# Kernel tuning notes

Hardware: AMD Instinct MI355X
Metric: run time of the kernel (lower is better)

## Reference

```python
import jax, jax.numpy as jnp
import numpy as np

N_NODES = 50000
N_EDGES = 800000
N_FEAT = 128
NHID = 64
B = 512          # num graphs
K = 30           # sort-pool k
N_CLASSES = 10


def _sage(x, src, dst, Wl, bl, Wr, n):
    # PyG SAGEConv: out = lin_l(mean_{j in N(i)} x_j) + lin_r(x_i)
    deg = jax.ops.segment_sum(jnp.ones(src.shape[0], x.dtype), dst, num_segments=n)
    agg = jax.ops.segment_sum(x[src], dst, num_segments=n)
    agg = agg / jnp.maximum(deg, 1.0)[:, None]
    return agg @ Wl + bl + x @ Wr


def _sort_pool(x, batch, num_graphs, k):
    # sort nodes within each graph descending by last feature channel, keep top-k (zero pad)
    n, f = x.shape
    order = jnp.lexsort((-x[:, -1], batch))  # primary: batch asc, secondary: last-feat desc
    xs = x[order]
    bs = batch[order]
    counts = jax.ops.segment_sum(jnp.ones(n, jnp.int32), batch, num_segments=num_graphs)
    starts = jnp.concatenate([jnp.zeros(1, jnp.int32), jnp.cumsum(counts)[:-1]])
    rank = jnp.arange(n, dtype=jnp.int32) - starts[bs]
    valid = rank < k
    gidx = jnp.where(valid, bs, num_graphs)  # out-of-bounds -> dropped by scatter
    ridx = jnp.where(valid, rank, 0)
    out = jnp.zeros((num_graphs, k, f), x.dtype).at[gidx, ridx].set(xs)
    return out  # [B, k, f]


def setup_inputs() -> dict:
    key = jax.random.key(0)
    ks = jax.random.split(key, 16)
    d = {}
    d["x"] = jax.random.normal(ks[0], (N_NODES, N_FEAT), dtype=jnp.float32)
    d["edge_index"] = jax.random.randint(ks[1], (2, N_EDGES), 0, N_NODES, dtype=jnp.int64)
    d["batch"] = jnp.sort(jax.random.randint(ks[2], (N_NODES,), 0, B, dtype=jnp.int64))

    def lin(k, fan_in, shape):
        s = 1.0 / np.sqrt(fan_in)
        return jax.random.uniform(k, shape, jnp.float32, -s, s)

    d["W1l"] = lin(ks[3], N_FEAT, (N_FEAT, NHID)); d["b1"] = lin(ks[4], N_FEAT, (NHID,))
    d["W1r"] = lin(ks[5], N_FEAT, (N_FEAT, NHID))
    d["W2l"] = lin(ks[6], NHID, (NHID, NHID)); d["b2"] = lin(ks[7], NHID, (NHID,))
    d["W2r"] = lin(ks[8], NHID, (NHID, NHID))
    d["W3l"] = lin(ks[9], NHID, (NHID, NHID)); d["b3"] = lin(ks[10], NHID, (NHID,))
    d["W3r"] = lin(ks[11], NHID, (NHID, NHID))
    d["convw"] = lin(ks[12], NHID * 5, (32, NHID, 5))  # OIH
    d["convb"] = lin(ks[13], NHID * 5, (32,))
    d["lin1w"] = lin(ks[14], 32 * 26, (32 * 26, NHID)); d["lin1b"] = lin(ks[14], 32 * 26, (NHID,))
    d["lin2w"] = lin(ks[15], NHID, (NHID, N_CLASSES)); d["lin2b"] = lin(ks[15], NHID, (N_CLASSES,))
    return d


def reference(x, edge_index, batch, W1l, b1, W1r, W2l, b2, W2r, W3l, b3, W3r,
              convw, convb, lin1w, lin1b, lin2w, lin2b):
    src, dst = edge_index[0], edge_index[1]
    h = jax.nn.relu(_sage(x, src, dst, W1l, b1, W1r, N_NODES))
    h = jax.nn.relu(_sage(h, src, dst, W2l, b2, W2r, N_NODES))
    h = jax.nn.relu(_sage(h, src, dst, W3l, b3, W3r, N_NODES))
    p = _sort_pool(h, batch, B, K)            # [B, K, NHID]
    p = jnp.transpose(p, (0, 2, 1))           # [B, NHID, K]
    c = jax.lax.conv_general_dilated(p, convw, (1,), 'VALID',
                                     dimension_numbers=('NCH', 'OIH', 'NCH'))
    c = jax.nn.relu(c + convb[None, :, None])  # [B, 32, 26]
    f = c.reshape(B, -1)
    f = jax.nn.relu(f @ lin1w + lin1b)
    logits = f @ lin2w + lin2b
    return jax.nn.log_softmax(logits, axis=-1)
```

## Files before the change

### kernel.cpp

```cpp
#include <hip/hip_runtime.h>
#include <hip/hip_bf16.h>
#include <math.h>

#define NND 50000
#define NE 800000
#define NF 128
#define NH 64
#define NB 512
#define KP 30
#define NCLS 10
#define NBKT 49
#define NTILE 196
#define NG1 782
#define NSET 208

typedef __hip_bfloat16 bf16;
typedef unsigned long long u64;
typedef unsigned short ushort_t;
typedef __attribute__((ext_vector_type(8))) short bf16x8;
typedef __attribute__((ext_vector_type(4))) float f32x4;

__device__ __forceinline__ float ldF(const void* p, size_t i, int isbf){
    return isbf ? __bfloat162float(((const bf16*)p)[i]) : ((const float*)p)[i];
}

__device__ __forceinline__ ushort_t f2bf(float v){
    unsigned u = __float_as_uint(v);
    unsigned r = u + 0x7FFFu + ((u >> 16) & 1u);
    return (ushort_t)(r >> 16);
}

__device__ __forceinline__ int floatsAreBf16(const unsigned* __restrict__ xw, int tid){
    unsigned w = xw[tid & 63];
    int ex = (int)((w >> 7) & 0xFF);
    u64 m = __ballot(ex >= 100 && ex <= 140);
    return __popcll(m) >= 32;
}
__device__ __forceinline__ int intsAreI64(const int* __restrict__ ew, int tid){
    u64 m = __ballot(ew[2*(tid & 63) + 1] == 0);
    return __popcll(m) >= 48;
}

__device__ __forceinline__ int edgeSrc(const int* ei, int e, int i64){
    return i64 ? ei[2*e] : ei[e];
}
__device__ __forceinline__ int edgeDst(const int* ei, int e, int i64){
    return i64 ? ei[2*NE + 2*e] : ei[NE + e];
}

__global__ __launch_bounds__(256) void k1_kernel(
    const unsigned* __restrict__ xw, const int* __restrict__ ei,
    const int* __restrict__ batch, int* __restrict__ starts,
    const void* W1l, const void* W1r, const void* b1,
    const void* W2l, const void* W2r, const void* b2,
    const void* W3l, const void* W3r, const void* b3,
    const void* convw, const void* convb,
    const void* l1w, const void* l1b, const void* l2w, const void* l2b,
    ushort_t* __restrict__ wB1, ushort_t* __restrict__ wB2, ushort_t* __restrict__ wB3,
    float* __restrict__ b1f, float* __restrict__ b2f, float* __restrict__ b3f,
    float* __restrict__ wT, float* __restrict__ cbf,
    float* __restrict__ l1wf, float* __restrict__ l1bf,
    float* __restrict__ l2wf, float* __restrict__ l2bf,
    int* __restrict__ bcnt, int* __restrict__ dctr,
    int* __restrict__ bbase, int* __restrict__ bcur, int* __restrict__ offs)
{
    int tid = threadIdx.x;
    if (blockIdx.x < NTILE){
        __shared__ int lh[NBKT];
        __shared__ int sc[NBKT];
        __shared__ int lastFlag;
        int i64 = intsAreI64(ei, tid);
        if (tid < NBKT) lh[tid] = 0;
        __syncthreads();
        int t0 = blockIdx.x*4096;
        #pragma unroll 4
        for (int k = 0; k < 16; ++k){
            int e = t0 + k*256 + tid;
            if (e < NE) atomicAdd(&lh[edgeDst(ei,e,i64) >> 10], 1);
        }
        __syncthreads();
        if (tid < NBKT && lh[tid]) atomicAdd(&bcnt[tid], lh[tid]);
        __syncthreads();
        if (tid == 0){
            __threadfence();
            int old = atomicAdd(dctr, 1);
            lastFlag = (old == NTILE-1) ? 1 : 0;
        }
        __syncthreads();
        if (lastFlag){
            if (tid < NBKT) sc[tid] = atomicAdd(&bcnt[tid], 0);
            __syncthreads();
            if (tid == 0){
                int acc = 0;
                for (int b = 0; b < NBKT; ++b){
                    bbase[b] = acc; bcur[b] = acc; acc += sc[b];
                }
                bbase[NBKT] = acc;
                offs[NND] = NE;
            }
        }
    } else {
        int wbf = floatsAreBf16(xw, tid);
        int i64 = intsAreI64(ei, tid);
        int i = (blockIdx.x - NTILE)*256 + tid;
        if (i < NND){
            int b  = i64 ? batch[2*i] : batch[i];
            int pb = (i == 0) ? -1 : (i64 ? batch[2*(i-1)] : batch[i-1]);
            for (int g = pb+1; g <= b; ++g) starts[g] = i;
            if (i == NND-1) for (int g = b+1; g <= NB; ++g) starts[g] = NND;
        }
        {
            int j = i & 7, lane = (i >> 3) & 63, t = (i >> 9) & 7, c = i >> 12;
            int k = c*32 + (lane >> 4)*8 + j;
            int n = t*16 + (lane & 15);
            if (i < 16384){
                float v = (n < 64) ? ldF(W1l, (size_t)k*NH + n, wbf)
                                   : ldF(W1r, (size_t)k*NH + (n-64), wbf);
                wB1[i] = f2bf(v);
            }
            if (i < 8192){
                float v2 = (n < 64) ? ldF(W2l, (size_t)k*NH + n, wbf)
                                    : ldF(W2r, (size_t)k*NH + (n-64), wbf);
                float v3 = (n < 64) ? ldF(W3l, (size_t)k*NH + n, wbf)
                                    : ldF(W3r, (size_t)k*NH + (n-64), wbf);
                wB2[i] = f2bf(v2);
                wB3[i] = f2bf(v3);
            }
        }
        if (i < 64){
            b1f[i] = ldF(b1, i, wbf);
            b2f[i] = ldF(b2, i, wbf);
            b3f[i] = ldF(b3, i, wbf);
            l1bf[i] = ldF(l1b, i, wbf);
        }
        if (i < 10240){
            int o = i / 320, rem = i - o*320, ch = rem/5, h = rem - ch*5;
            wT[ch*160 + h*32 + o] = ldF(convw, i, wbf);
        }
        if (i < 53248) l1wf[i] = ldF(l1w, i, wbf);
        if (i < 640)   l2wf[i] = ldF(l2w, i, wbf);
        if (i < 32)    cbf[i]  = ldF(convb, i, wbf);
        if (i < 10)    l2bf[i] = ldF(l2b, i, wbf);
    }
}

__global__ __launch_bounds__(256) void k2_kernel(
    const void* __restrict__ x, const int* __restrict__ ei,
    const ushort_t* __restrict__ wB1, const float* __restrict__ b1f,
    ushort_t* __restrict__ ybf, float* __restrict__ z,
    int* __restrict__ bcur, int2* __restrict__ bedges)
{
    int tid = threadIdx.x;
    if (blockIdx.x < NG1){
        constexpr int K = NF, KC = K/32, RS = K + 8;
        __shared__ ushort_t hA[64*RS];
        int isbf = floatsAreBf16((const unsigned*)x, tid);
        int base = blockIdx.x * 64;
        for (int i = tid; i < 64*K; i += 256){
            int r = i / K, c = i - r*K;
            int node = base + r;
            float v = (node < NND) ? ldF(x, (size_t)node*K + c, isbf) : 0.f;
            hA[r*RS + c] = f2bf(v);
        }
        __syncthreads();
        int lane = tid & 63, w = tid >> 6;
        int n16 = lane & 15, quad = lane >> 4;
        f32x4 acc[8];
        #pragma unroll
        for (int t = 0; t < 8; ++t) acc[t] = (f32x4){0.f,0.f,0.f,0.f};
        const bf16x8* bp = (const bf16x8*)wB1;
        #pragma unroll
        for (int c = 0; c < KC; ++c){
            bf16x8 a = *(const bf16x8*)&hA[(w*16 + n16)*RS + c*32 + quad*8];
            #pragma unroll
            for (int t = 0; t < 8; ++t){
                bf16x8 b = bp[(c*8 + t)*64 + lane];
                acc[t] = __builtin_amdgcn_mfma_f32_16x16x32_bf16(a, b, acc[t], 0, 0, 0);
            }
        }
        #pragma unroll
        for (int t = 0; t < 8; ++t){
            int f = (t & 3)*16 + n16;
            float bv = (t >= 4) ? b1f[f] : 0.f;
            #pragma unroll
            for (int r = 0; r < 4; ++r){
                int node = base + w*16 + quad*4 + r;
                if (node < NND){
                    if (t < 4) ybf[(size_t)node*NH + f] = f2bf(acc[t][r]);
                    else       z[(size_t)node*NH + f] = acc[t][r] + bv;
                }
            }
        }
    } else {
        __shared__ int lh[NBKT];
        __shared__ int lcur[NBKT];
        int i64 = intsAreI64(ei, tid);
        if (tid < NBKT) lh[tid] = 0;
        __syncthreads();
        int t0 = (blockIdx.x - NG1)*4096;
        int myd[16], mys[16];
        int cnt = 0;
        #pragma unroll 4
        for (int k = 0; k < 16; ++k){
            int e = t0 + k*256 + tid;
            if (e < NE){
                int d = edgeDst(ei,e,i64), s_ = edgeSrc(ei,e,i64);
                myd[cnt] = d; mys[cnt] = s_; ++cnt;
                atomicAdd(&lh[d >> 10], 1);
            }
        }
        __syncthreads();
        if (tid < NBKT) lcur[tid] = lh[tid] ? atomicAdd(&bcur[tid], lh[tid]) : 0;
        __syncthreads();
        for (int k = 0; k < cnt; ++k){
            int b = myd[k] >> 10;
            int p = atomicAdd(&lcur[b], 1);
            bedges[p] = make_int2(mys[k], myd[k]);
        }
    }
}

__global__ __launch_bounds__(1024) void csr_finalize(const int2* __restrict__ bedges,
                                                     const int* __restrict__ bbase,
                                                     int* __restrict__ offs,
                                                     int* __restrict__ csr){
    __shared__ int hist[1024];
    int b = blockIdx.x;
    int tid = threadIdx.x;
    int dst0 = b << 10;
    int nd = NND - dst0; if (nd > 1024) nd = 1024;
    int e0 = bbase[b], e1 = bbase[b+1];
    hist[tid] = 0;
    __syncthreads();
    for (int e = e0 + tid; e < e1; e += 1024)
        atomicAdd(&hist[bedges[e].y - dst0], 1);
    __syncthreads();
    int own = hist[tid];
    for (int st = 1; st < 1024; st <<= 1){
        int v = (tid >= st) ? hist[tid-st] : 0;
        __syncthreads();
        hist[tid] += v;
        __syncthreads();
    }
    int excl = hist[tid] - own;
    if (tid < nd) offs[dst0 + tid] = e0 + excl;
    __syncthreads();
    hist[tid] = excl;
    __syncthreads();
    for (int e = e0 + tid; e < e1; e += 1024){
        int2 ed = bedges[e];
        int p = atomicAdd(&hist[ed.y - dst0], 1);
        csr[e0 + p] = ed.x;
    }
}

__device__ __forceinline__ void addbf8(uint4 u, float* a){
    a[0] += __uint_as_float(u.x << 16);
    a[1] += __uint_as_float(u.x & 0xFFFF0000u);
    a[2] += __uint_as_float(u.y << 16);
    a[3] += __uint_as_float(u.y & 0xFFFF0000u);
    a[4] += __uint_as_float(u.z << 16);
    a[5] += __uint_as_float(u.z & 0xFFFF0000u);
    a[6] += __uint_as_float(u.w << 16);
    a[7] += __uint_as_float(u.w & 0xFFFF0000u);
}

__global__ __launch_bounds__(256) void gather_mfma(
    const ushort_t* __restrict__ yb, const int* __restrict__ offs,
    const int* __restrict__ csr, const float* __restrict__ z,
    const ushort_t* __restrict__ wB, const float* __restrict__ bfp,
    ushort_t* __restrict__ ybf_out, float* __restrict__ z_out,
    ushort_t* __restrict__ ykey_out)
{
    constexpr int K = NH;
    constexpr int KC = K/32;
    constexpr int RS = K + 8;
    __shared__ ushort_t hA[64*RS];
    int tid = threadIdx.x;
    int base = blockIdx.x * 64;

    {
        int nl = tid >> 2, q = tid & 3;
        int node = base + nl;
        float acc[16];
        #pragma unroll
        for (int i = 0; i < 16; ++i) acc[i] = 0.f;
        ushort_t row[16];
        if (node < NND){
            int o0 = offs[node], o1 = offs[node+1];
            int e = o0;
            for (; e + 3 < o1; e += 4){
                int s0 = csr[e], s1 = csr[e+1], s2 = csr[e+2], s3 = csr[e+3];
                const uint4* p0 = (const uint4*)&yb[(size_t)s0*NH + q*16];
                const uint4* p1 = (const uint4*)&yb[(size_t)s1*NH + q*16];
                const uint4* p2 = (const uint4*)&yb[(size_t)s2*NH + q*16];
                const uint4* p3 = (const uint4*)&yb[(size_t)s3*NH + q*16];
                uint4 a0 = p0[0], a1 = p0[1], b0 = p1[0], b1 = p1[1];
                uint4 c0 = p2[0], c1 = p2[1], d0 = p3[0], d1 = p3[1];
                addbf8(a0, acc); addbf8(a1, acc+8);
                addbf8(b0, acc); addbf8(b1, acc+8);
                addbf8(c0, acc); addbf8(c1, acc+8);
                addbf8(d0, acc); addbf8(d1, acc+8);
            }
            for (; e < o1; ++e){
                const uint4* p0 = (const uint4*)&yb[(size_t)csr[e]*NH + q*16];
                uint4 a0 = p0[0], a1 = p0[1];
                addbf8(a0, acc); addbf8(a1, acc+8);
            }
            float dd = (float)(o1 - o0); dd = dd > 1.f ? dd : 1.f;
            float inv = 1.f / dd;
            const float4* zp = (const float4*)&z[(size_t)node*NH + q*16];
            #pragma unroll
            for (int i4 = 0; i4 < 4; ++i4){
                float4 zz = zp[i4];
                float v0 = acc[i4*4+0]*inv + zz.x;
                float v1 = acc[i4*4+1]*inv + zz.y;
                float v2 = acc[i4*4+2]*inv + zz.z;
                float v3 = acc[i4*4+3]*inv + zz.w;
                row[i4*4+0] = f2bf(v0 > 0.f ? v0 : 0.f);
                row[i4*4+1] = f2bf(v1 > 0.f ? v1 : 0.f);
                row[i4*4+2] = f2bf(v2 > 0.f ? v2 : 0.f);
                row[i4*4+3] = f2bf(v3 > 0.f ? v3 : 0.f);
            }
        } else {
            #pragma unroll
            for (int i = 0; i < 16; ++i) row[i] = 0;
        }
        unsigned pk[8];
        #pragma unroll
        for (int i = 0; i < 8; ++i)
            pk[i] = (unsigned)row[2*i] | ((unsigned)row[2*i+1] << 16);
        *(uint4*)&hA[nl*RS + q*16]     = make_uint4(pk[0],pk[1],pk[2],pk[3]);
        *(uint4*)&hA[nl*RS + q*16 + 8] = make_uint4(pk[4],pk[5],pk[6],pk[7]);
    }
    __syncthreads();

    int lane = tid & 63, w = tid >> 6;
    int n16 = lane & 15, quad = lane >> 4;
    f32x4 acc[8];
    #pragma unroll
    for (int t = 0; t < 8; ++t) acc[t] = (f32x4){0.f,0.f,0.f,0.f};
    const bf16x8* bp = (const bf16x8*)wB;
    #pragma unroll
    for (int c = 0; c < KC; ++c){
        bf16x8 a = *(const bf16x8*)&hA[(w*16 + n16)*RS + c*32 + quad*8];
        #pragma unroll
        for (int t = 0; t < 8; ++t){
            bf16x8 b = bp[(c*8 + t)*64 + lane];
            acc[t] = __builtin_amdgcn_mfma_f32_16x16x32_bf16(a, b, acc[t], 0, 0, 0);
        }
    }
    #pragma unroll
    for (int t = 0; t < 8; ++t){
        int f = (t & 3)*16 + n16;
        float bv = (t >= 4) ? bfp[f] : 0.f;
        #pragma unroll
        for (int r = 0; r < 4; ++r){
            int node = base + w*16 + quad*4 + r;
            if (node < NND){
                if (t < 4){
                    ushort_t yv = f2bf(acc[t][r]);
                    ybf_out[(size_t)node*NH + f] = yv;
                    if (ykey_out != nullptr && t == 3 && n16 == 15)
                        ykey_out[node] = yv;
                } else {
                    z_out[(size_t)node*NH + f] = acc[t][r] + bv;
                }
            }
        }
    }
}

__device__ __forceinline__ void acc4(uint2 u, float& a0, float& a1, float& a2, float& a3){
    a0 += __uint_as_float(u.x << 16);
    a1 += __uint_as_float(u.x & 0xFFFF0000u);
    a2 += __uint_as_float(u.y << 16);
    a3 += __uint_as_float(u.y & 0xFFFF0000u);
}

__device__ __forceinline__ u64 shflx64(u64 v, int m){
    int lo = __shfl_xor((int)(unsigned)v, m, 64);
    int hi = __shfl_xor((int)(unsigned)(v >> 32), m, 64);
    return ((u64)(unsigned)hi << 32) | (unsigned)lo;
}

#define PSTR 33
__global__ __launch_bounds__(512, 4) void head4_kernel(
    const ushort_t* __restrict__ yb, const ushort_t* __restrict__ ykey,
    const int* __restrict__ offs, const int* __restrict__ csr,
    const float* __restrict__ z, const int* __restrict__ starts,
    const float* __restrict__ wT, const float* __restrict__ cbf,
    const float* __restrict__ l1wf, const float* __restrict__ l1bf,
    const float* __restrict__ l2wf, const float* __restrict__ l2bf,
    float* __restrict__ outp)
{
    __shared__ u64  keysL[512];
    __shared__ int  sel[32];
    __shared__ float pT[64*PSTR];
    __shared__ float part[8*832];
    __shared__ float cbuf[832];
    __shared__ float fbuf[NH];
    __shared__ float logitsS[NCLS];
    int g = blockIdx.x, tid = threadIdx.x;
    int s = starts[g], e = starts[g+1];
    int cnt = e - s; if (cnt > 256) cnt = 256; if (cnt < 0) cnt = 0;

    u64 key = 0xFFFFFFFFFFFFFFFFull;
    if (tid < cnt){
        int node = s + tid;
        int o0 = offs[node], o1 = offs[node+1];
        float a = 0.f;
        int ee = o0;
        for (; ee + 3 < o1; ee += 4){
            float v0 = __uint_as_float((unsigned)ykey[csr[ee+0]] << 16);
            float v1 = __uint_as_float((unsigned)ykey[csr[ee+1]] << 16);
            float v2 = __uint_as_float((unsigned)ykey[csr[ee+2]] << 16);
            float v3 = __uint_as_float((unsigned)ykey[csr[ee+3]] << 16);
            a += v0; a += v1; a += v2; a += v3;
        }
        for (; ee < o1; ++ee)
            a += __uint_as_float((unsigned)ykey[csr[ee]] << 16);
        float dd = (float)(o1 - o0); dd = dd > 1.f ? dd : 1.f;
        float inv = 1.f / dd;
        float v = a*inv + z[(size_t)node*NH + 63];
        v = v > 0.f ? v : 0.f;
        unsigned u = __float_as_uint(v);
        unsigned m = (u & 0x80000000u) ? ~u : (u | 0x80000000u);
        unsigned d = ~m;
        key = ((u64)d << 32) | (unsigned)tid;
    }

    for (int k = 2; k <= 256; k <<= 1){
        for (int j = k >> 1; j > 0; j >>= 1){
            u64 other;
            if (j >= 64){
                keysL[tid] = key;
                __syncthreads();
                other = keysL[tid ^ j];
            } else {
                other = shflx64(key, j);
            }
            bool keepMin = (((tid & j) == 0) == ((tid & k) == 0));
            bool less = key < other;
            key = (keepMin == less) ? key : other;
            if (j >= 64) __syncthreads();
        }
    }
    if (tid < KP)
        sel[tid] = (((unsigned)(key >> 32)) == 0xFFFFFFFFu) ? -1 : (int)(key & 0xFFFFFFFFu);
    __syncthreads();

    {
        int r = tid >> 4;
        int q = tid & 15;
        if (r < KP){
            float4 v = make_float4(0.f,0.f,0.f,0.f);
            int li = sel[r];
            if (li >= 0){
                int node = s + li;
                int o0 = offs[node], o1 = offs[node+1];
                float a0=0.f, a1=0.f, a2=0.f, a3=0.f;
                int ee = o0;
                for (; ee + 3 < o1; ee += 4){
                    int s0 = csr[ee], s1 = csr[ee+1], s2 = csr[ee+2], s3 = csr[ee+3];
                    uint2 u0 = *(const uint2*)&yb[(size_t)s0*NH + q*4];
                    uint2 u1 = *(const uint2*)&yb[(size_t)s1*NH + q*4];
                    uint2 u2 = *(const uint2*)&yb[(size_t)s2*NH + q*4];
                    uint2 u3 = *(const uint2*)&yb[(size_t)s3*NH + q*4];
                    acc4(u0, a0,a1,a2,a3); acc4(u1, a0,a1,a2,a3);
                    acc4(u2, a0,a1,a2,a3); acc4(u3, a0,a1,a2,a3);
                }
                for (; ee < o1; ++ee){
                    uint2 u = *(const uint2*)&yb[(size_t)csr[ee]*NH + q*4];
                    acc4(u, a0,a1,a2,a3);
                }
                float dd = (float)(o1 - o0); dd = dd > 1.f ? dd : 1.f;
                float inv = 1.f / dd;
                float4 zz = *(const float4*)&z[(size_t)node*NH + q*4];
                v.x = a0*inv + zz.x; v.y = a1*inv + zz.y;
                v.z = a2*inv + zz.z; v.w = a3*inv + zz.w;
                v.x = v.x > 0.f ? v.x : 0.f;  v.y = v.y > 0.f ? v.y : 0.f;
                v.z = v.z > 0.f ? v.z : 0.f;  v.w = v.w > 0.f ? v.w : 0.f;
            }
            pT[(q*4+0)*PSTR + r] = v.x;
            pT[(q*4+1)*PSTR + r] = v.y;
            pT[(q*4+2)*PSTR + r] = v.z;
            pT[(q*4+3)*PSTR + r] = v.w;
        }
    }
    __syncthreads();

    {
        int o = tid & 31, th = (tid >> 5) & 1, chg = tid >> 6;
        int tbase = th*13;
        float acc[13];
        #pragma unroll
        for (int t = 0; t < 13; ++t) acc[t] = 0.f;
        for (int c8 = 0; c8 < 8; ++c8){
            int ch = chg*8 + c8;
            float p[17];
            #pragma unroll
            for (int i = 0; i < 17; ++i) p[i] = pT[ch*PSTR + tbase + i];
            const float* wrow = &wT[ch*160 + o];
            #pragma unroll
            for (int h = 0; h < 5; ++h){
                float wv = wrow[h*32];
                #pragma unroll
                for (int t = 0; t < 13; ++t) acc[t] += p[t+h]*wv;
            }
        }
        #pragma unroll
        for (int t = 0; t < 13; ++t) part[chg*832 + o*26 + tbase + t] = acc[t];
    }
    __syncthreads();

    for (int i = tid; i < 832; i += 512){
        int oo = i / 26;
        float a = cbf[oo];
        #pragma unroll
        for (int cg = 0; cg < 8; ++cg) a += part[cg*832 + i];
        cbuf[i] = a > 0.f ? a : 0.f;
    }
    __syncthreads();

    {
        int p8 = tid >> 6, j = tid & 63;
        float a = 0.f;
        int m0 = p8*104;
        #pragma unroll 4
        for (int m = m0; m < m0 + 104; ++m)
            a += cbuf[m] * l1wf[(size_t)m*NH + j];
        part[p8*NH + j] = a;
    }
    __syncthreads();
    if (tid < NH){
        float v = part[tid];
        #pragma unroll
        for (int p8 = 1; p8 < 8; ++p8) v += part[p8*NH + tid];
        v += l1bf[tid];
        fbuf[tid] = v > 0.f ? v : 0.f;
    }
    __syncthreads();
    if (tid < NCLS){
        float a = l2bf[tid];
        #pragma unroll
        for (int j = 0; j < NH; ++j) a += fbuf[j] * l2wf[j*NCLS + tid];
        logitsS[tid] = a;
    }
    __syncthreads();
    if (tid == 0){
        float m = logitsS[0];
        for (int c = 1; c < NCLS; ++c) m = fmaxf(m, logitsS[c]);
        float ssum = 0.f;
        for (int c = 0; c < NCLS; ++c) ssum += expf(logitsS[c]-m);
        float lse = m + logf(ssum);
        for (int c = 0; c < NCLS; ++c)
            outp[(size_t)g*NCLS + c] = logitsS[c] - lse;
    }
}

extern "C" void kernel_launch(void* const* d_in, const int* in_sizes, int n_in,
                              void* d_out, int out_size, void* d_ws, size_t ws_size,
                              hipStream_t stream) {
    const void* x    = d_in[0];
    const int*  ei   = (const int*)d_in[1];
    const int*  batch= (const int*)d_in[2];
    const void *W1l=d_in[3], *b1=d_in[4],  *W1r=d_in[5];
    const void *W2l=d_in[6], *b2=d_in[7],  *W2r=d_in[8];
    const void *W3l=d_in[9], *b3=d_in[10], *W3r=d_in[11];
    const void *convw=d_in[12], *convb=d_in[13];
    const void *l1w=d_in[14], *l1b=d_in[15];
    const void *l2w=d_in[16], *l2b=d_in[17];
    float* out = (float*)d_out;

    float* wsf = (float*)d_ws;
    ushort_t* yA = (ushort_t*)wsf;
    float* zA  = wsf + (size_t)NND*NH/2;
    ushort_t* yB = (ushort_t*)(zA + (size_t)NND*NH);
    float* zB  = (float*)(yB + (size_t)NND*NH);
    int2* bedges = (int2*)(zB + (size_t)NND*NH);
    ushort_t* wB1 = (ushort_t*)(bedges + NE);
    ushort_t* wB2 = wB1 + 16384;
    ushort_t* wB3 = wB2 + 8192;
    ushort_t* ykey = wB3 + 8192;
    float* b1f  = (float*)(ykey + NND + 8);
    float* b2f  = b1f + 64;
    float* b3f  = b2f + 64;
    float* wT   = b3f + 64;
    float* cbf  = wT + 10240;
    float* l1wf = cbf + 32;
    float* l1bf = l1wf + 53248;
    float* l2wf = l1bf + 64;
    float* l2bf = l2wf + 640;
    int* starts = (int*)(l2bf + 16);
    int* bcnt   = starts + 520;
    int* dctr   = bcnt + NBKT;
    int* bbase  = bcnt + 64;
    int* bcur   = bbase + 64;
    int* offs   = bcur + 64;
    int* csr    = offs + NND + 3;

    (void)hipMemsetAsync(bcnt, 0, 50*sizeof(int), stream);

    k1_kernel<<<NTILE + NSET, 256, 0, stream>>>(
        (const unsigned*)x, ei, batch, starts,
        W1l, W1r, b1, W2l, W2r, b2, W3l, W3r, b3,
        convw, convb, l1w, l1b, l2w, l2b,
        wB1, wB2, wB3, b1f, b2f, b3f,
        wT, cbf, l1wf, l1bf, l2wf, l2bf,
        bcnt, dctr, bbase, bcur, offs);

    k2_kernel<<<NG1 + NTILE, 256, 0, stream>>>(
        x, ei, wB1, b1f, yA, zA, bcur, bedges);

    csr_finalize<<<NBKT, 1024, 0, stream>>>(bedges, bbase, offs, csr);

    gather_mfma<<<NG1, 256, 0, stream>>>(yA, offs, csr, zA, wB2, b2f, yB, zB, nullptr);
    gather_mfma<<<NG1, 256, 0, stream>>>(yB, offs, csr, zB, wB3, b3f, yA, zA, ykey);

    head4_kernel<<<NB, 512, 0, stream>>>(yA, ykey, offs, csr, zA, starts,
                                         wT, cbf, l1wf, l1bf, l2wf, l2bf, out);
}
```

Before: 247.7 us.

## Refine CSR buckets, vectorize edge/feature loads, widen gather blocks to 512 threads

Switches the CSR build from 49 buckets of 1024 destinations to 196 buckets of 256, so csr_finalize runs more, smaller 256-thread blocks. Edge loads are vectorized as int4 pairs in the int64 case. The first-layer x tile is staged into shared memory with 16-byte vector loads and packed bf16 conversion. gather_mfma now uses 512 threads, with 8 lanes per node for the neighbour gather and the 8 MFMA column tiles split across two wave groups, trading more per-block parallelism for extra launch/occupancy pressure.

Result: faster. 222.4 us (-10.2%).

```diff
diff --git a/kernel.cpp b/kernel.cpp
--- a/kernel.cpp
+++ b/kernel.cpp
@@ -9,7 +9,8 @@
 #define NB 512
 #define KP 30
 #define NCLS 10
-#define NBKT 49
+#define NBKT 196
+#define BSH 8
 #define NTILE 196
 #define NG1 782
 #define NSET 208
@@ -73,10 +74,22 @@
         if (tid < NBKT) lh[tid] = 0;
         __syncthreads();
         int t0 = blockIdx.x*4096;
-        #pragma unroll 4
-        for (int k = 0; k < 16; ++k){
-            int e = t0 + k*256 + tid;
-            if (e < NE) atomicAdd(&lh[edgeDst(ei,e,i64) >> 10], 1);
+        if (i64){
+            #pragma unroll 4
+            for (int k = 0; k < 8; ++k){
+                int e = t0 + k*512 + 2*tid;
+                if (e < NE){
+                    int4 dp = *(const int4*)&ei[2*NE + 2*e];
+                    atomicAdd(&lh[dp.x >> BSH], 1);
+                    atomicAdd(&lh[dp.z >> BSH], 1);
+                }
+            }
+        } else {
+            #pragma unroll 4
+            for (int k = 0; k < 16; ++k){
+                int e = t0 + k*256 + tid;
+                if (e < NE) atomicAdd(&lh[ei[NE + e] >> BSH], 1);
+            }
         }
         __syncthreads();
         if (tid < NBKT && lh[tid]) atomicAdd(&bcnt[tid], lh[tid]);
@@ -156,11 +169,30 @@
         __shared__ ushort_t hA[64*RS];
         int isbf = floatsAreBf16((const unsigned*)x, tid);
         int base = blockIdx.x * 64;
-        for (int i = tid; i < 64*K; i += 256){
-            int r = i / K, c = i - r*K;
-            int node = base + r;
-            float v = (node < NND) ? ldF(x, (size_t)node*K + c, isbf) : 0.f;
-            hA[r*RS + c] = f2bf(v);
+        if (isbf){
+            for (int j = tid; j < 64*K/8; j += 256){
+                int r = j >> 4, c8 = (j & 15)*8;
+                int node = base + r;
+                uint4 v = make_uint4(0u,0u,0u,0u);
+                if (node < NND)
+                    v = *(const uint4*)((const ushort_t*)x + (size_t)node*K + c8);
+                *(uint4*)&hA[r*RS + c8] = v;
+            }
+        } else {
+            for (int j = tid; j < 64*K/8; j += 256){
+                int r = j >> 4, c8 = (j & 15)*8;
+                int node = base + r;
+                uint4 pk = make_uint4(0u,0u,0u,0u);
+                if (node < NND){
+                    const float4* xp = (const float4*)((const float*)x + (size_t)node*K + c8);
+                    float4 a = xp[0], b = xp[1];
+                    pk.x = (unsigned)f2bf(a.x) | ((unsigned)f2bf(a.y) << 16);
+                    pk.y = (unsigned)f2bf(a.z) | ((unsigned)f2bf(a.w) << 16);
+                    pk.z = (unsigned)f2bf(b.x) | ((unsigned)f2bf(b.y) << 16);
+                    pk.w = (unsigned)f2bf(b.z) | ((unsigned)f2bf(b.w) << 16);
+                }
+                *(uint4*)&hA[r*RS + c8] = pk;
+            }
         }
         __syncthreads();
         int lane = tid & 63, w = tid >> 6;
@@ -200,43 +232,58 @@
         int t0 = (blockIdx.x - NG1)*4096;
         int myd[16], mys[16];
         int cnt = 0;
-        #pragma unroll 4
-        for (int k = 0; k < 16; ++k){
-            int e = t0 + k*256 + tid;
-            if (e < NE){
-                int d = edgeDst(ei,e,i64), s_ = edgeSrc(ei,e,i64);
-                myd[cnt] = d; mys[cnt] = s_; ++cnt;
-                atomicAdd(&lh[d >> 10], 1);
+        if (i64){
+            #pragma unroll 4
+            for (int k = 0; k < 8; ++k){
+                int e = t0 + k*512 + 2*tid;
+                if (e < NE){
+                    int4 sp = *(const int4*)&ei[2*e];
+                    int4 dp = *(const int4*)&ei[2*NE + 2*e];
+                    myd[cnt] = dp.x; mys[cnt] = sp.x; ++cnt;
+                    atomicAdd(&lh[dp.x >> BSH], 1);
+                    myd[cnt] = dp.z; mys[cnt] = sp.z; ++cnt;
+                    atomicAdd(&lh[dp.z >> BSH], 1);
+                }
+            }
+        } else {
+            #pragma unroll 4
+            for (int k = 0; k < 16; ++k){
+                int e = t0 + k*256 + tid;
+                if (e < NE){
+                    int d = ei[NE + e], s_ = ei[e];
+                    myd[cnt] = d; mys[cnt] = s_; ++cnt;
+                    atomicAdd(&lh[d >> BSH], 1);
+                }
             }
         }
         __syncthreads();
         if (tid < NBKT) lcur[tid] = lh[tid] ? atomicAdd(&bcur[tid], lh[tid]) : 0;
         __syncthreads();
         for (int k = 0; k < cnt; ++k){
-            int b = myd[k] >> 10;
+            int b = myd[k] >> BSH;
             int p = atomicAdd(&lcur[b], 1);
             bedges[p] = make_int2(mys[k], myd[k]);
         }
     }
 }
 
-__global__ __launch_bounds__(1024) void csr_finalize(const int2* __restrict__ bedges,
-                                                     const int* __restrict__ bbase,
-                                                     int* __restrict__ offs,
-                                                     int* __restrict__ csr){
-    __shared__ int hist[1024];
+__global__ __launch_bounds__(256) void csr_finalize(const int2* __restrict__ bedges,
+                                                    const int* __restrict__ bbase,
+                                                    int* __restrict__ offs,
+                                                    int* __restrict__ csr){
+    __shared__ int hist[256];
     int b = blockIdx.x;
     int tid = threadIdx.x;
-    int dst0 = b << 10;
-    int nd = NND - dst0; if (nd > 1024) nd = 1024;
+    int dst0 = b << BSH;
+    int nd = NND - dst0; if (nd > 256) nd = 256;
     int e0 = bbase[b], e1 = bbase[b+1];
     hist[tid] = 0;
     __syncthreads();
-    for (int e = e0 + tid; e < e1; e += 1024)
+    for (int e = e0 + tid; e < e1; e += 256)
         atomicAdd(&hist[bedges[e].y - dst0], 1);
     __syncthreads();
     int own = hist[tid];
-    for (int st = 1; st < 1024; st <<= 1){
+    for (int st = 1; st < 256; st <<= 1){
         int v = (tid >= st) ? hist[tid-st] : 0;
         __syncthreads();
         hist[tid] += v;
@@ -247,7 +294,7 @@
     __syncthreads();
     hist[tid] = excl;
     __syncthreads();
-    for (int e = e0 + tid; e < e1; e += 1024){
+    for (int e = e0 + tid; e < e1; e += 256){
         int2 ed = bedges[e];
         int p = atomicAdd(&hist[ed.y - dst0], 1);
         csr[e0 + p] = ed.x;
@@ -265,7 +312,7 @@
     a[7] += __uint_as_float(u.w & 0xFFFF0000u);
 }
 
-__global__ __launch_bounds__(256) void gather_mfma(
+__global__ __launch_bounds__(512) void gather_mfma(
     const ushort_t* __restrict__ yb, const int* __restrict__ offs,
     const int* __restrict__ csr, const float* __restrict__ z,
     const ushort_t* __restrict__ wB, const float* __restrict__ bfp,
@@ -280,38 +327,32 @@
     int base = blockIdx.x * 64;
 
     {
-        int nl = tid >> 2, q = tid & 3;
+        int nl = tid >> 3, q = tid & 7;
         int node = base + nl;
-        float acc[16];
-        #pragma unroll
-        for (int i = 0; i < 16; ++i) acc[i] = 0.f;
-        ushort_t row[16];
+        float acc[8];
+        #pragma unroll
+        for (int i = 0; i < 8; ++i) acc[i] = 0.f;
+        ushort_t row[8];
         if (node < NND){
             int o0 = offs[node], o1 = offs[node+1];
             int e = o0;
             for (; e + 3 < o1; e += 4){
                 int s0 = csr[e], s1 = csr[e+1], s2 = csr[e+2], s3 = csr[e+3];
-                const uint4* p0 = (const uint4*)&yb[(size_t)s0*NH + q*16];
-                const uint4* p1 = (const uint4*)&yb[(size_t)s1*NH + q*16];
-                const uint4* p2 = (const uint4*)&yb[(size_t)s2*NH + q*16];
-                const uint4* p3 = (const uint4*)&yb[(size_t)s3*NH + q*16];
-                uint4 a0 = p0[0], a1 = p0[1], b0 = p1[0], b1 = p1[1];
-                uint4 c0 = p2[0], c1 = p2[1], d0 = p3[0], d1 = p3[1];
-                addbf8(a0, acc); addbf8(a1, acc+8);
-                addbf8(b0, acc); addbf8(b1, acc+8);
-                addbf8(c0, acc); addbf8(c1, acc+8);
-                addbf8(d0, acc); addbf8(d1, acc+8);
+                uint4 a0 = *(const uint4*)&yb[(size_t)s0*NH + q*8];
+                uint4 b0 = *(const uint4*)&yb[(size_t)s1*NH + q*8];
+                uint4 c0 = *(const uint4*)&yb[(size_t)s2*NH + q*8];
+                uint4 d0 = *(const uint4*)&yb[(size_t)s3*NH + q*8];
+                addbf8(a0, acc); addbf8(b0, acc); addbf8(c0, acc); addbf8(d0, acc);
             }
             for (; e < o1; ++e){
-                const uint4* p0 = (const uint4*)&yb[(size_t)csr[e]*NH + q*16];
-                uint4 a0 = p0[0], a1 = p0[1];
-                addbf8(a0, acc); addbf8(a1, acc+8);
+                uint4 a0 = *(const uint4*)&yb[(size_t)csr[e]*NH + q*8];
+                addbf8(a0, acc);
             }
             float dd = (float)(o1 - o0); dd = dd > 1.f ? dd : 1.f;
             float inv = 1.f / dd;
-            const float4* zp = (const float4*)&z[(size_t)node*NH + q*16];
-            #pragma unroll
-            for (int i4 = 0; i4 < 4; ++i4){
+            const float4* zp = (const float4*)&z[(size_t)node*NH + q*8];
+            #pragma unroll
+            for (int i4 = 0; i4 < 2; ++i4){
                 float4 zz = zp[i4];
                 float v0 = acc[i4*4+0]*inv + zz.x;
                 float v1 = acc[i4*4+1]*inv + zz.y;
@@ -324,48 +365,58 @@
             }
         } else {
             #pragma unroll
-            for (int i = 0; i < 16; ++i) row[i] = 0;
-        }
-        unsigned pk[8];
-        #pragma unroll
-        for (int i = 0; i < 8; ++i)
+            for (int i = 0; i < 8; ++i) row[i] = 0;
+        }
+        unsigned pk[4];
+        #pragma unroll
+        for (int i = 0; i < 4; ++i)
             pk[i] = (unsigned)row[2*i] | ((unsigned)row[2*i+1] << 16);
-        *(uint4*)&hA[nl*RS + q*16]     = make_uint4(pk[0],pk[1],pk[2],pk[3]);
-        *(uint4*)&hA[nl*RS + q*16 + 8] = make_uint4(pk[4],pk[5],pk[6],pk[7]);
-    }
-    __syncthreads();
-
-    int lane = tid & 63, w = tid >> 6;
+        *(uint4*)&hA[nl*RS + q*8] = make_uint4(pk[0],pk[1],pk[2],pk[3]);
+    }
+    __syncthreads();
+
+    int lane = tid & 63, w8 = tid >> 6;
+    int wrow = w8 & 3;
+    int thalf = (w8 >> 2) << 2;
     int n16 = lane & 15, quad = lane >> 4;
-    f32x4 acc[8];
+    f32x4 acc[4];
     #pragma unroll
-    for (int t = 0; t < 8; ++t) acc[t] = (f32x4){0.f,0.f,0.f,0.f};
+    for (int t = 0; t < 4; ++t) acc[t] = (f32x4){0.f,0.f,0.f,0.f};
     const bf16x8* bp = (const bf16x8*)wB;
     #pragma unroll
     for (int c = 0; c < KC; ++c){
-        bf16x8 a = *(const bf16x8*)&hA[(w*16 + n16)*RS + c*32 + quad*8];
-        #pragma unroll
-        for (int t = 0; t < 8; ++t){
-            bf16x8 b = bp[(c*8 + t)*64 + lane];
-            acc[t] = __builtin_amdgcn_mfma_f32_16x16x32_bf16(a, b, acc[t], 0, 0, 0);
-        }
-    }
-    #pragma unroll
-    for (int t = 0; t < 8; ++t){
-        int f = (t & 3)*16 + n16;
-        float bv = (t >= 4) ? bfp[f] : 0.f;
-        #pragma unroll
-        for (int r = 0; r < 4; ++r){
-            int node = base + w*16 + quad*4 + r;
-            if (node < NND){
-                if (t < 4){
-                    ushort_t yv = f2bf(acc[t][r]);
+        bf16x8 a = *(const bf16x8*)&hA[(wrow*16 + n16)*RS + c*32 + quad*8];
+        #pragma unroll
+        for (int tt = 0; tt < 4; ++tt){
+            bf16x8 b = bp[(c*8 + thalf + tt)*64 + lane];
+            acc[tt] = __builtin_amdgcn_mfma_f32_16x16x32_bf16(a, b, acc[tt], 0, 0, 0);
+        }
+    }
+    if (thalf == 0){
+        #pragma unroll
+        for (int tt = 0; tt < 4; ++tt){
+            int f = tt*16 + n16;
+            #pragma unroll
+            for (int r = 0; r < 4; ++r){
+                int node = base + wrow*16 + quad*4 + r;
+                if (node < NND){
+                    ushort_t yv = f2bf(acc[tt][r]);
                     ybf_out[(size_t)node*NH + f] = yv;
-                    if (ykey_out != nullptr && t == 3 && n16 == 15)
+                    if (ykey_out != nullptr && tt == 3 && n16 == 15)
                         ykey_out[node] = yv;
-                } else {
-                    z_out[(size_t)node*NH + f] = acc[t][r] + bv;
-                }
+                }
+            }
+        }
+    } else {
+        #pragma unroll
+        for (int tt = 0; tt < 4; ++tt){
+            int f = tt*16 + n16;
+            float bv = bfp[f];
+            #pragma unroll
+            for (int r = 0; r < 4; ++r){
+                int node = base + wrow*16 + quad*4 + r;
+                if (node < NND)
+                    z_out[(size_t)node*NH + f] = acc[tt][r] + bv;
             }
         }
     }
@@ -595,12 +646,12 @@
     int* starts = (int*)(l2bf + 16);
     int* bcnt   = starts + 520;
     int* dctr   = bcnt + NBKT;
-    int* bbase  = bcnt + 64;
-    int* bcur   = bbase + 64;
-    int* offs   = bcur + 64;
+    int* bbase  = bcnt + 208;
+    int* bcur   = bbase + 208;
+    int* offs   = bcur + 208;
     int* csr    = offs + NND + 3;
 
-    (void)hipMemsetAsync(bcnt, 0, 50*sizeof(int), stream);
+    (void)hipMemsetAsync(bcnt, 0, (NBKT+1)*sizeof(int), stream);
 
     k1_kernel<<<NTILE + NSET, 256, 0, stream>>>(
         (const unsigned*)x, ei, batch, starts,
@@ -613,10 +664,10 @@
     k2_kernel<<<NG1 + NTILE, 256, 0, stream>>>(
         x, ei, wB1, b1f, yA, zA, bcur, bedges);
 
-    csr_finalize<<<NBKT, 1024, 0, stream>>>(bedges, bbase, offs, csr);
-
-    gather_mfma<<<NG1, 256, 0, stream>>>(yA, offs, csr, zA, wB2, b2f, yB, zB, nullptr);
-    gather_mfma<<<NG1, 256, 0, stream>>>(yB, offs, csr, zB, wB3, b3f, yA, zA, ykey);
+    csr_finalize<<<NBKT, 256, 0, stream>>>(bedges, bbase, offs, csr);
+
+    gather_mfma<<<NG1, 512, 0, stream>>>(yA, offs, csr, zA, wB2, b2f, yB, zB, nullptr);
+    gather_mfma<<<NG1, 512, 0, stream>>>(yB, offs, csr, zB, wB3, b3f, yA, zA, ykey);
 
     head4_kernel<<<NB, 512, 0, stream>>>(yA, ykey, offs, csr, zA, starts,
                                          wT, cbf, l1wf, l1bf, l2wf, l2bf, out);
```
